# Kernel optimization log

Hardware: AMD Instinct MI355X
Metric: run time of the kernel (lower is better)

Reference implementation:

```python
import jax, jax.numpy as jnp
import numpy as np

# Constants derived from init_kwargs: dt, simulation_params = [gamma, omega, n, eta, kappa, b]
DT = 0.001
GAMMA, OMEGA, N_TH, ETA, KAPPA = 0.3, 6.283185, 14.0, 0.8, 0.9
A = jnp.array([[-GAMMA / 2, OMEGA], [-OMEGA, -GAMMA / 2]], dtype=jnp.float32)
C = np.float32(np.sqrt(4 * ETA * KAPPA)) * jnp.array([[1.0, 0.0], [0.0, 0.0]], dtype=jnp.float32)
D = np.float32(GAMMA * (N_TH + 0.5) + KAPPA) * jnp.eye(2, dtype=jnp.float32)
PROJ_F = jnp.array([[0.0, 0.0], [1.0, 0.0]], dtype=jnp.float32)  # squeezed proj_F

B, T = 4096, 2048


def setup_inputs() -> dict:
    key = jax.random.key(0)
    k1, k2, k3 = jax.random.split(key, 3)
    dy = jax.random.normal(k1, (B, T, 2), dtype=jnp.float32) * np.float32(np.sqrt(DT))
    state = jax.random.uniform(k2, (B, 6), dtype=jnp.float32)  # [q, p, Vx, Vp, Cxp, t]
    f = jax.random.normal(k3, (B, 2), dtype=jnp.float32)
    kernel_params = jnp.array([[0.0, 1.0], [-1.0, 0.0]], dtype=jnp.float32)  # trainable 2x2
    return {"dy": dy, "state": state, "f": f, "kernel_params": kernel_params}


def _step(state, f, dy_t, K):
    # state: [B,6], f: [B,2], dy_t: [B,2], K: [2,2]
    x = state[:, :2]
    vx, vp, cxp = state[:, 2], state[:, 3], state[:, 4]
    t = state[:, 5]
    cov = jnp.stack([jnp.stack([vx, cxp], -1), jnp.stack([cxp, vp], -1)], -2)  # [B,2,2]
    xicov = jnp.einsum('bij,kj->bik', cov, C)  # cov @ C.T
    M = A[None] - jnp.einsum('bij,jk->bik', xicov, C)  # A - xicov @ C
    dx = jnp.einsum('bij,bj->bi', M, x) * DT + jnp.einsum('bij,bj->bi', xicov, dy_t)
    fnew = f + jnp.einsum('ij,bj->bi', K, f) * DT
    dx = dx + jnp.einsum('ij,bj->bi', PROJ_F, fnew) * DT
    ncov = cov + DT * (
        jnp.einsum('bij,kj->bik', cov, A)
        + jnp.einsum('ij,bjk->bik', A, cov)
        + D[None]
        - jnp.einsum('bij,bkj->bik', xicov, xicov)
    )
    nstate = jnp.concatenate(
        [x + dx, ncov[:, 0, 0:1], ncov[:, 1, 1:2], ncov[:, 1, 0:1], (t + DT)[:, None]], axis=1
    )
    dy_hat = jnp.einsum('ij,bj->bi', C, x) * DT  # uses OLD x, as in torch code
    return nstate, fnew, dy_hat


def reference(dy, state, f, kernel_params):
    dy_tb = jnp.swapaxes(dy, 0, 1)  # [T,B,2]

    def scan_fn(carry, dyt):
        s, fc = carry
        ns, fn, yh = _step(s, fc, dyt, kernel_params)
        return (ns, fn), yh

    (nstate, fnew), dy_hat = jax.lax.scan(scan_fn, (state, f), dy_tb)
    return nstate, jnp.swapaxes(dy_hat, 0, 1), fnew
```

## Files before the change

kernel.cpp:

```cpp
#include <hip/hip_runtime.h>
#include <cmath>


#define NBATCH 4096
#define NT     2048
#define ROWF4  1024

struct M16 { float m[16]; };

namespace gk {

constexpr float DT   = 0.001f;
constexpr float A00  = -0.15f;
constexpr float A01  = 6.283185f;
constexpr float A10  = -6.283185f;
constexpr float A11  = -0.15f;
constexpr float C0   = 1.6970562748477141f;
constexpr float DD   = 5.25f;

constexpr float P00c = 1.0f + DT*A00;
constexpr float P01c = DT*A01;
constexpr float P10c = DT*A10;
constexpr float P11c = 1.0f + DT*A11;
constexpr float DTC  = DT*C0;
constexpr float QQ   = DT*C0*C0;
constexpr float cVA  = 1.0f + 2.0f*DT*A00;
constexpr float cVB  = 2.0f*DT*A01;
constexpr float cVBn = 2.0f*DT*A10;
constexpr float cVD  = DT*DD;
constexpr float cCA  = 1.0f + DT*(A00+A11);
constexpr float cCB  = DT*A10;
constexpr float cCC  = DT*A01;
constexpr float YC   = C0*DT;

__device__ __forceinline__ void cov_step(float& vx, float& vp, float& cxp)
{
    float a1 = fmaf(-QQ, vx,  cVA);
    float b1 = fmaf(cVB, cxp, cVD);
    float a2 = fmaf(-QQ, cxp, cVBn);
    float b2 = fmaf(a2,  cxp, cVD);
    float a3 = fmaf(-QQ, vx,  cCA);
    float m  = cCC * vp;
    float c3 = fmaf(cCB, vx,  m);
    float nvx = fmaf(a1,  vx,  b1);
    float nvp = fmaf(cVA, vp,  b2);
    float ncx = fmaf(a3,  cxp, c3);
    vx = nvx; vp = nvp; cxp = ncx;
}

__device__ __forceinline__ void covf_step(
    float& vx, float& vp, float& cxp, float& f0, float& f1,
    float k00, float k01, float k10, float k11,
    float& xi0o, float& xi1o, float& nf0o)
{
    float xi0 = C0*vx, xi1 = C0*cxp;
    float nf0 = fmaf(DT, fmaf(k00, f0, k01*f1), f0);
    float nf1 = fmaf(DT, fmaf(k10, f0, k11*f1), f1);
    xi0o = xi0; xi1o = xi1; nf0o = nf0;
    cov_step(vx, vp, cxp);
    f0 = nf0; f1 = nf1;
}

__device__ __forceinline__ void mat4_mul(const float* A, const float* B, float* C)
{
    #pragma unroll
    for (int i = 0; i < 4; ++i)
        #pragma unroll
        for (int j = 0; j < 4; ++j) {
            float acc = A[i*4+0] * B[0*4+j];
            acc = fmaf(A[i*4+1], B[1*4+j], acc);
            acc = fmaf(A[i*4+2], B[2*4+j], acc);
            acc = fmaf(A[i*4+3], B[3*4+j], acc);
            C[i*4+j] = acc;
        }
}

__device__ __forceinline__ void lft_apply(const float* m, float& vx, float& vp, float& cxp)
{
    float n00 = fmaf(m[0], vx,  fmaf(m[1], cxp, m[2]));
    float n01 = fmaf(m[0], cxp, fmaf(m[1], vp,  m[3]));
    float n10 = fmaf(m[4], vx,  fmaf(m[5], cxp, m[6]));
    float n11 = fmaf(m[4], cxp, fmaf(m[5], vp,  m[7]));
    float d00 = fmaf(m[8],  vx,  fmaf(m[9],  cxp, m[10]));
    float d01 = fmaf(m[8],  cxp, fmaf(m[9],  vp,  m[11]));
    float d10 = fmaf(m[12], vx,  fmaf(m[13], cxp, m[14]));
    float d11 = fmaf(m[12], cxp, fmaf(m[13], vp,  m[15]));
    float rdet = 1.0f / fmaf(d00, d11, -d01*d10);
    float p00 = fmaf(n00, d11, -n01*d10) * rdet;
    float p01 = fmaf(n01, d00, -n00*d01) * rdet;
    float p10 = fmaf(n10, d11, -n11*d10) * rdet;
    float p11 = fmaf(n11, d00, -n10*d01) * rdet;
    vx = p00; vp = p11; cxp = 0.5f*(p01 + p10);
}

__device__ __forceinline__ void seg_checkpoint(
    const M16& ml, int s,
    float k00, float k01, float k10, float k11,
    float& vx, float& vp, float& cxp, float& f0, float& f1)
{
    float acc[16] = {1,0,0,0, 0,1,0,0, 0,0,1,0, 0,0,0,1};
    float bas[16];
    #pragma unroll
    for (int i = 0; i < 16; ++i) bas[i] = ml.m[i];
    #pragma unroll
    for (int it = 0; it < 6; ++it) {
        float t[16];
        if ((s >> it) & 1) {
            mat4_mul(acc, bas, t);
            #pragma unroll
            for (int i = 0; i < 16; ++i) acc[i] = t[i];
        }
        if (it < 5) {
            mat4_mul(bas, bas, t);
            #pragma unroll
            for (int i = 0; i < 16; ++i) bas[i] = t[i];
        }
    }
    lft_apply(acc, vx, vp, cxp);

    float m00 = fmaf(DT,k00,1.f), m01 = DT*k01;
    float m10 = DT*k10,           m11 = fmaf(DT,k11,1.f);
    #pragma unroll
    for (int i = 0; i < 5; ++i) {
        float a = fmaf(m00,m00, m01*m10);
        float q = fmaf(m00,m01, m01*m11);
        float c = fmaf(m10,m00, m11*m10);
        float d = fmaf(m10,m01, m11*m11);
        m00=a; m01=q; m10=c; m11=d;
    }
    float a00=1.f, a01=0.f, a10=0.f, a11=1.f;
    #pragma unroll
    for (int it = 0; it < 6; ++it) {
        if ((s >> it) & 1) {
            float x0 = fmaf(a00,m00, a01*m10);
            float x1 = fmaf(a00,m01, a01*m11);
            float x2 = fmaf(a10,m00, a11*m10);
            float x3 = fmaf(a10,m01, a11*m11);
            a00=x0; a01=x1; a10=x2; a11=x3;
        }
        if (it < 5) {
            float x0 = fmaf(m00,m00, m01*m10);
            float x1 = fmaf(m00,m01, m01*m11);
            float x2 = fmaf(m10,m00, m11*m10);
            float x3 = fmaf(m10,m01, m11*m11);
            m00=x0; m01=x1; m10=x2; m11=x3;
        }
    }
    float nf0 = fmaf(a00, f0, a01*f1);
    float nf1 = fmaf(a10, f0, a11*f1);
    f0 = nf0; f1 = nf1;
}

__device__ __forceinline__ int xcd_swz(int bx, int n)
{
    return (bx & 7) * (n >> 3) + (bx >> 3);
}

}

__global__ void __launch_bounds__(256, 3)
kfused(const float* __restrict__ dy, const float* __restrict__ state,
       const float* __restrict__ fin, const float* __restrict__ kp,
       M16 mc, float* __restrict__ out)
{
    using namespace gk;
    const int lane = threadIdx.x & 63;
    const int wv   = threadIdx.x >> 6;
    const int g    = xcd_swz(blockIdx.x, gridDim.x);
    const int b    = g*4 + wv;
    const int s    = lane;

    const float k00 = kp[0], k01 = kp[1], k10 = kp[2], k11 = kp[3];
    const float x0i = state[b*6+0], x1i = state[b*6+1];
    const float vx0 = state[b*6+2], vp0 = state[b*6+3], cx0 = state[b*6+4];
    const float t0  = state[b*6+5];
    const float f0i = fin[b*2+0],   f1i = fin[b*2+1];

    const float4* base = reinterpret_cast<const float4*>(dy)
                       + (size_t)b*ROWF4 + s*16;
    float4 v[16];
    #pragma unroll
    for (int j = 0; j < 16; ++j) v[j] = base[j];

    float vx = vx0, vp = vp0, cxp = cx0, f0 = f0i, f1 = f1i;
    seg_checkpoint(mc, s, k00, k01, k10, k11, vx, vp, cxp, f0, f1);
    const float vxs = vx, vps = vp, cxs = cxp, f0s = f0, f1s = f1;

    float X00 = 1.f, X01 = 0.f, X10 = 0.f, X11 = 1.f, Q0 = 0.f, Q1 = 0.f;
    #pragma unroll
    for (int j = 0; j < 16; ++j) {
        #pragma unroll
        for (int h = 0; h < 2; ++h) {
            float dy0 = h ? v[j].z : v[j].x;
            float xi0, xi1, nf0;
            covf_step(vx, vp, cxp, f0, f1, k00, k01, k10, k11, xi0, xi1, nf0);
            float p00 = fmaf(-DTC, xi0, P00c);
            float p10 = fmaf(-DTC, xi1, P10c);
            float r0  = xi0*dy0;
            float r1  = fmaf(DT, nf0, xi1*dy0);
            float nX00 = fmaf(p00, X00, P01c*X10);
            float nX01 = fmaf(p00, X01, P01c*X11);
            float nX10 = fmaf(p10, X00, P11c*X10);
            float nX11 = fmaf(p10, X01, P11c*X11);
            float nQ0  = fmaf(p00, Q0, fmaf(P01c, Q1, r0));
            float nQ1  = fmaf(p10, Q0, fmaf(P11c, Q1, r1));
            X00 = nX00; X01 = nX01; X10 = nX10; X11 = nX11; Q0 = nQ0; Q1 = nQ1;
        }
    }

    float A00 = X00, A01 = X01, A10 = X10, A11 = X11, B0 = Q0, B1 = Q1;
    #pragma unroll
    for (int d = 1; d < 64; d <<= 1) {
        float r00 = __shfl_up(A00, d);
        float r01 = __shfl_up(A01, d);
        float r10 = __shfl_up(A10, d);
        float r11 = __shfl_up(A11, d);
        float rB0 = __shfl_up(B0,  d);
        float rB1 = __shfl_up(B1,  d);
        if (lane >= d) {
            float n00 = fmaf(A00, r00, A01*r10);
            float n01 = fmaf(A00, r01, A01*r11);
            float n10 = fmaf(A10, r00, A11*r10);
            float n11 = fmaf(A10, r01, A11*r11);
            float nB0 = fmaf(A00, rB0, fmaf(A01, rB1, B0));
            float nB1 = fmaf(A10, rB0, fmaf(A11, rB1, B1));
            A00=n00; A01=n01; A10=n10; A11=n11; B0=nB0; B1=nB1;
        }
    }
    float e00 = __shfl_up(A00, 1);
    float e01 = __shfl_up(A01, 1);
    float e10 = __shfl_up(A10, 1);
    float e11 = __shfl_up(A11, 1);
    float eB0 = __shfl_up(B0,  1);
    float eB1 = __shfl_up(B1,  1);
    float x0 = (s == 0) ? x0i : fmaf(e00, x0i, fmaf(e01, x1i, eB0));
    float x1 = (s == 0) ? x1i : fmaf(e10, x0i, fmaf(e11, x1i, eB1));

    vx = vxs; vp = vps; cxp = cxs; f0 = f0s; f1 = f1s;
    #pragma unroll
    for (int j = 0; j < 16; ++j) {
        float yh0, yh1;
        #pragma unroll
        for (int h = 0; h < 2; ++h) {
            float dy0 = h ? v[j].z : v[j].x;
            float yh  = YC * x0;
            if (h) yh1 = yh; else yh0 = yh;
            float xi0, xi1, nf0;
            covf_step(vx, vp, cxp, f0, f1, k00, k01, k10, k11, xi0, xi1, nf0);
            float p00 = fmaf(-DTC, xi0, P00c);
            float p10 = fmaf(-DTC, xi1, P10c);
            float r0  = xi0*dy0;
            float r1  = fmaf(DT, nf0, xi1*dy0);
            float nx0 = fmaf(p00, x0, fmaf(P01c, x1, r0));
            float nx1 = fmaf(p10, x0, fmaf(P11c, x1, r1));
            x0 = nx0; x1 = nx1;
        }
        v[j] = make_float4(yh0, 0.f, yh1, 0.f);
    }

    float4* dst = reinterpret_cast<float4*>(out + 6*NBATCH)
                + (size_t)b*ROWF4 + s*16;
    #pragma unroll
    for (int j = 0; j < 16; ++j) dst[j] = v[j];

    if (s == 63) {
        out[b*6+0] = x0; out[b*6+1] = x1;
        out[b*6+2] = vx; out[b*6+3] = vp; out[b*6+4] = cxp;
        out[b*6+5] = t0 + 2.048f;
        float* fo = out + 6*NBATCH + (size_t)NBATCH*NT*2;
        fo[b*2+0] = f0; fo[b*2+1] = f1;
    }
}

static M16 build_m_pow(int log2l)
{
    const double dt = 0.001;
    const double a00 = -0.15, a01 = 6.283185, a10 = -6.283185, a11 = -0.15;
    const double qq = dt * 4.0 * 0.8 * 0.9;
    const double qd = dt * 5.25;
    const double h00 = 1.0 + dt*a00, h01 = dt*a01;
    const double h10 = dt*a10,       h11 = 1.0 + dt*a11;
    const double det = h00*h11 - h01*h10;
    const double t00 = h11/det, t01 = -h10/det, t10 = -h01/det, t11 = h00/det;
    const double g00 = t00*qq, g10 = t10*qq;
    double M[4][4] = {
        { h00 + qd*g00, h01, qd*t00, qd*t01 },
        { h10 + qd*g10, h11, qd*t10, qd*t11 },
        { g00,          0.0, t00,    t01    },
        { g10,          0.0, t10,    t11    },
    };
    for (int it = 0; it < log2l; ++it) {
        double R[4][4];
        for (int i = 0; i < 4; ++i)
            for (int j = 0; j < 4; ++j) {
                double acc = 0.0;
                for (int k = 0; k < 4; ++k) acc += M[i][k]*M[k][j];
                R[i][j] = acc;
            }
        for (int i = 0; i < 4; ++i)
            for (int j = 0; j < 4; ++j) M[i][j] = R[i][j];
    }
    M16 r;
    for (int i = 0; i < 4; ++i)
        for (int j = 0; j < 4; ++j) r.m[i*4+j] = (float)M[i][j];
    return r;
}

extern "C" void kernel_launch(void* const* d_in, const int* in_sizes, int n_in,
                              void* d_out, int out_size, void* d_ws, size_t ws_size,
                              hipStream_t stream)
{
    const float* dy    = (const float*)d_in[0];
    const float* state = (const float*)d_in[1];
    const float* fin   = (const float*)d_in[2];
    const float* kp    = (const float*)d_in[3];
    float* out = (float*)d_out;

    M16 mc = build_m_pow(5);

    kfused<<<dim3(NBATCH/4), dim3(256), 0, stream>>>(dy, state, fin, kp, mc, out);
}
```

Measured before the change: 43.55 us.

## Split each batch row across two wavefronts with shared-memory prefix handoff

Each batch row was previously handled by one 64-lane wave, with each lane covering 32 timesteps. Now two waves share a row, each lane covers 16 timesteps, and the second half starts from a covariance and f checkpoint computed from a precomputed 1024-step power matrix. Wave 0's affine prefix total passes to wave 1 through shared memory after a block barrier. This halves the sequential per-thread chain and register footprint, raising the occupancy hint from 3 to 6. The cost is twice as many checkpoint computations and an added __syncthreads, and the large-power checkpoint may be less accurate.

```diff
diff --git a/kernel.cpp b/kernel.cpp
--- a/kernel.cpp
+++ b/kernel.cpp
@@ -93,102 +93,111 @@
     vx = p00; vp = p11; cxp = 0.5f*(p01 + p10);
 }
 
-__device__ __forceinline__ void seg_checkpoint(
-    const M16& ml, int s,
-    float k00, float k01, float k10, float k11,
-    float& vx, float& vp, float& cxp, float& f0, float& f1)
-{
-    float acc[16] = {1,0,0,0, 0,1,0,0, 0,0,1,0, 0,0,0,1};
-    float bas[16];
-    #pragma unroll
-    for (int i = 0; i < 16; ++i) bas[i] = ml.m[i];
-    #pragma unroll
-    for (int it = 0; it < 6; ++it) {
-        float t[16];
-        if ((s >> it) & 1) {
-            mat4_mul(acc, bas, t);
+__device__ __forceinline__ int xcd_swz(int bx, int n)
+{
+    return (bx & 7) * (n >> 3) + (bx >> 3);
+}
+
+}
+
+__global__ void __launch_bounds__(256, 6)
+kfused(const float* __restrict__ dy, const float* __restrict__ state,
+       const float* __restrict__ fin, const float* __restrict__ kp,
+       M16 ml, M16 mh, float* __restrict__ out)
+{
+    using namespace gk;
+    __shared__ float tsh[2][8];
+    const int lane = threadIdx.x & 63;
+    const int wv   = threadIdx.x >> 6;
+    const int bi   = wv >> 1;
+    const int w    = wv & 1;
+    const int g    = xcd_swz(blockIdx.x, gridDim.x);
+    const int b    = g*2 + bi;
+
+    const float k00 = kp[0], k01 = kp[1], k10 = kp[2], k11 = kp[3];
+    const float x0i = state[b*6+0], x1i = state[b*6+1];
+    const float vx0 = state[b*6+2], vp0 = state[b*6+3], cx0 = state[b*6+4];
+    const float t0v = state[b*6+5];
+    const float f0i = fin[b*2+0],   f1i = fin[b*2+1];
+
+    float vx = vx0, vp = vp0, cxp = cx0;
+    {
+        float acc[16] = {1,0,0,0, 0,1,0,0, 0,0,1,0, 0,0,0,1};
+        float bas[16];
+        #pragma unroll
+        for (int i = 0; i < 16; ++i) bas[i] = ml.m[i];
+        #pragma unroll
+        for (int it = 0; it < 6; ++it) {
+            float t[16];
+            if ((lane >> it) & 1) {
+                mat4_mul(acc, bas, t);
+                #pragma unroll
+                for (int i = 0; i < 16; ++i) acc[i] = t[i];
+            }
+            if (it < 5) {
+                mat4_mul(bas, bas, t);
+                #pragma unroll
+                for (int i = 0; i < 16; ++i) bas[i] = t[i];
+            }
+        }
+        if (w) {
+            float t[16];
+            mat4_mul(acc, mh.m, t);
             #pragma unroll
             for (int i = 0; i < 16; ++i) acc[i] = t[i];
         }
-        if (it < 5) {
-            mat4_mul(bas, bas, t);
-            #pragma unroll
-            for (int i = 0; i < 16; ++i) bas[i] = t[i];
-        }
-    }
-    lft_apply(acc, vx, vp, cxp);
-
-    float m00 = fmaf(DT,k00,1.f), m01 = DT*k01;
-    float m10 = DT*k10,           m11 = fmaf(DT,k11,1.f);
-    #pragma unroll
-    for (int i = 0; i < 5; ++i) {
-        float a = fmaf(m00,m00, m01*m10);
-        float q = fmaf(m00,m01, m01*m11);
-        float c = fmaf(m10,m00, m11*m10);
-        float d = fmaf(m10,m01, m11*m11);
-        m00=a; m01=q; m10=c; m11=d;
-    }
-    float a00=1.f, a01=0.f, a10=0.f, a11=1.f;
-    #pragma unroll
-    for (int it = 0; it < 6; ++it) {
-        if ((s >> it) & 1) {
+        lft_apply(acc, vx, vp, cxp);
+    }
+    float f0 = f0i, f1 = f1i;
+    {
+        float m00 = fmaf(DT,k00,1.f), m01 = DT*k01;
+        float m10 = DT*k10,           m11 = fmaf(DT,k11,1.f);
+        #pragma unroll
+        for (int i = 0; i < 4; ++i) {
+            float a = fmaf(m00,m00, m01*m10);
+            float q = fmaf(m00,m01, m01*m11);
+            float c = fmaf(m10,m00, m11*m10);
+            float d = fmaf(m10,m01, m11*m11);
+            m00=a; m01=q; m10=c; m11=d;
+        }
+        float a00=1.f, a01=0.f, a10=0.f, a11=1.f;
+        #pragma unroll
+        for (int it = 0; it < 6; ++it) {
+            if ((lane >> it) & 1) {
+                float x0 = fmaf(a00,m00, a01*m10);
+                float x1 = fmaf(a00,m01, a01*m11);
+                float x2 = fmaf(a10,m00, a11*m10);
+                float x3 = fmaf(a10,m01, a11*m11);
+                a00=x0; a01=x1; a10=x2; a11=x3;
+            }
+            float x0 = fmaf(m00,m00, m01*m10);
+            float x1 = fmaf(m00,m01, m01*m11);
+            float x2 = fmaf(m10,m00, m11*m10);
+            float x3 = fmaf(m10,m01, m11*m11);
+            m00=x0; m01=x1; m10=x2; m11=x3;
+        }
+        if (w) {
             float x0 = fmaf(a00,m00, a01*m10);
             float x1 = fmaf(a00,m01, a01*m11);
             float x2 = fmaf(a10,m00, a11*m10);
             float x3 = fmaf(a10,m01, a11*m11);
             a00=x0; a01=x1; a10=x2; a11=x3;
         }
-        if (it < 5) {
-            float x0 = fmaf(m00,m00, m01*m10);
-            float x1 = fmaf(m00,m01, m01*m11);
-            float x2 = fmaf(m10,m00, m11*m10);
-            float x3 = fmaf(m10,m01, m11*m11);
-            m00=x0; m01=x1; m10=x2; m11=x3;
-        }
-    }
-    float nf0 = fmaf(a00, f0, a01*f1);
-    float nf1 = fmaf(a10, f0, a11*f1);
-    f0 = nf0; f1 = nf1;
-}
-
-__device__ __forceinline__ int xcd_swz(int bx, int n)
-{
-    return (bx & 7) * (n >> 3) + (bx >> 3);
-}
-
-}
-
-__global__ void __launch_bounds__(256, 3)
-kfused(const float* __restrict__ dy, const float* __restrict__ state,
-       const float* __restrict__ fin, const float* __restrict__ kp,
-       M16 mc, float* __restrict__ out)
-{
-    using namespace gk;
-    const int lane = threadIdx.x & 63;
-    const int wv   = threadIdx.x >> 6;
-    const int g    = xcd_swz(blockIdx.x, gridDim.x);
-    const int b    = g*4 + wv;
-    const int s    = lane;
-
-    const float k00 = kp[0], k01 = kp[1], k10 = kp[2], k11 = kp[3];
-    const float x0i = state[b*6+0], x1i = state[b*6+1];
-    const float vx0 = state[b*6+2], vp0 = state[b*6+3], cx0 = state[b*6+4];
-    const float t0  = state[b*6+5];
-    const float f0i = fin[b*2+0],   f1i = fin[b*2+1];
+        float nf0 = fmaf(a00, f0, a01*f1);
+        float nf1 = fmaf(a10, f0, a11*f1);
+        f0 = nf0; f1 = nf1;
+    }
+    const float vxs = vx, vps = vp, cxs = cxp, f0s = f0, f1s = f1;
 
     const float4* base = reinterpret_cast<const float4*>(dy)
-                       + (size_t)b*ROWF4 + s*16;
-    float4 v[16];
-    #pragma unroll
-    for (int j = 0; j < 16; ++j) v[j] = base[j];
-
-    float vx = vx0, vp = vp0, cxp = cx0, f0 = f0i, f1 = f1i;
-    seg_checkpoint(mc, s, k00, k01, k10, k11, vx, vp, cxp, f0, f1);
-    const float vxs = vx, vps = vp, cxs = cxp, f0s = f0, f1s = f1;
+                       + (size_t)b*ROWF4 + w*512 + lane*8;
+    float4 v[8];
+    #pragma unroll
+    for (int j = 0; j < 8; ++j) v[j] = base[j];
 
     float X00 = 1.f, X01 = 0.f, X10 = 0.f, X11 = 1.f, Q0 = 0.f, Q1 = 0.f;
     #pragma unroll
-    for (int j = 0; j < 16; ++j) {
+    for (int j = 0; j < 8; ++j) {
         #pragma unroll
         for (int h = 0; h < 2; ++h) {
             float dy0 = h ? v[j].z : v[j].x;
@@ -227,18 +236,32 @@
             A00=n00; A01=n01; A10=n10; A11=n11; B0=nB0; B1=nB1;
         }
     }
+
+    if (w == 0 && lane == 63) {
+        tsh[bi][0]=A00; tsh[bi][1]=A01; tsh[bi][2]=A10;
+        tsh[bi][3]=A11; tsh[bi][4]=B0;  tsh[bi][5]=B1;
+    }
+    __syncthreads();
+    float xb0 = x0i, xb1 = x1i;
+    if (w == 1) {
+        float T00=tsh[bi][0], T01=tsh[bi][1], T10=tsh[bi][2];
+        float T11=tsh[bi][3], TB0=tsh[bi][4], TB1=tsh[bi][5];
+        xb0 = fmaf(T00, x0i, fmaf(T01, x1i, TB0));
+        xb1 = fmaf(T10, x0i, fmaf(T11, x1i, TB1));
+    }
+
     float e00 = __shfl_up(A00, 1);
     float e01 = __shfl_up(A01, 1);
     float e10 = __shfl_up(A10, 1);
     float e11 = __shfl_up(A11, 1);
     float eB0 = __shfl_up(B0,  1);
     float eB1 = __shfl_up(B1,  1);
-    float x0 = (s == 0) ? x0i : fmaf(e00, x0i, fmaf(e01, x1i, eB0));
-    float x1 = (s == 0) ? x1i : fmaf(e10, x0i, fmaf(e11, x1i, eB1));
+    float x0 = (lane == 0) ? xb0 : fmaf(e00, xb0, fmaf(e01, xb1, eB0));
+    float x1 = (lane == 0) ? xb1 : fmaf(e10, xb0, fmaf(e11, xb1, eB1));
 
     vx = vxs; vp = vps; cxp = cxs; f0 = f0s; f1 = f1s;
     #pragma unroll
-    for (int j = 0; j < 16; ++j) {
+    for (int j = 0; j < 8; ++j) {
         float yh0, yh1;
         #pragma unroll
         for (int h = 0; h < 2; ++h) {
@@ -259,20 +282,20 @@
     }
 
     float4* dst = reinterpret_cast<float4*>(out + 6*NBATCH)
-                + (size_t)b*ROWF4 + s*16;
-    #pragma unroll
-    for (int j = 0; j < 16; ++j) dst[j] = v[j];
-
-    if (s == 63) {
+                + (size_t)b*ROWF4 + w*512 + lane*8;
+    #pragma unroll
+    for (int j = 0; j < 8; ++j) dst[j] = v[j];
+
+    if (w == 1 && lane == 63) {
         out[b*6+0] = x0; out[b*6+1] = x1;
         out[b*6+2] = vx; out[b*6+3] = vp; out[b*6+4] = cxp;
-        out[b*6+5] = t0 + 2.048f;
+        out[b*6+5] = t0v + 2.048f;
         float* fo = out + 6*NBATCH + (size_t)NBATCH*NT*2;
         fo[b*2+0] = f0; fo[b*2+1] = f1;
     }
 }
 
-static M16 build_m_pow(int log2l)
+static M16 build_m_pow(int log2n)
 {
     const double dt = 0.001;
     const double a00 = -0.15, a01 = 6.283185, a10 = -6.283185, a11 = -0.15;
@@ -289,7 +312,7 @@
         { g00,          0.0, t00,    t01    },
         { g10,          0.0, t10,    t11    },
     };
-    for (int it = 0; it < log2l; ++it) {
+    for (int it = 0; it < log2n; ++it) {
         double R[4][4];
         for (int i = 0; i < 4; ++i)
             for (int j = 0; j < 4; ++j) {
@@ -316,7 +339,8 @@
     const float* kp    = (const float*)d_in[3];
     float* out = (float*)d_out;
 
-    M16 mc = build_m_pow(5);
-
-    kfused<<<dim3(NBATCH/4), dim3(256), 0, stream>>>(dy, state, fin, kp, mc, out);
-}
+    M16 ml = build_m_pow(4);
+    M16 mh = build_m_pow(10);
+
+    kfused<<<dim3(NBATCH/2), dim3(256), 0, stream>>>(dy, state, fin, kp, ml, mh, out);
+}
```

Result: slower. 67.35 us (+54.7%).
